# Optimization experiments

Hardware: AMD Instinct MI355X
Metric: run time of the kernel (lower is better)

Reference implementation:

```python
import jax, jax.numpy as jnp
import numpy as np

B, P, E = 128, 196, 2048      # batch, num_pixels (14x14), encoder_dim
A = D = EMB = 512             # attention_dim, decoder_dim, embed_dim
V = 18022                     # vocab_size
MAXLEN = 52                   # max caption length; decode steps T = MAXLEN-1


def _lin(key, fan_in, fan_out):
    k1, k2 = jax.random.split(key)
    s = 1.0 / np.sqrt(fan_in)
    W = jax.random.uniform(k1, (fan_in, fan_out), minval=-s, maxval=s, dtype=jnp.float32)
    b = jax.random.uniform(k2, (fan_out,), minval=-s, maxval=s, dtype=jnp.float32)
    return W, b


def setup_inputs() -> dict:
    key = jax.random.key(0)
    ks = jax.random.split(key, 14)
    W_enc_att, b_enc_att = _lin(ks[0], E, A)
    W_dec_att, b_dec_att = _lin(ks[1], D, A)
    w_full, b_full = _lin(ks[2], A, 1)
    W_init_h, b_init_h = _lin(ks[3], E, D)
    W_init_c, b_init_c = _lin(ks[4], E, D)
    W_fbeta, b_fbeta = _lin(ks[5], D, E)
    # LSTMCell params (torch layout: [4D, in] / [4D, D], gate order i,f,g,o)
    s = 1.0 / np.sqrt(D)
    W_ih = jax.random.uniform(ks[6], (4 * D, EMB + E), minval=-s, maxval=s, dtype=jnp.float32)
    W_hh = jax.random.uniform(ks[7], (4 * D, D), minval=-s, maxval=s, dtype=jnp.float32)
    b_ih = jax.random.uniform(ks[8], (4 * D,), minval=-s, maxval=s, dtype=jnp.float32)
    b_hh = jax.random.uniform(ks[9], (4 * D,), minval=-s, maxval=s, dtype=jnp.float32)
    # embedding and fc initialized uniform(-0.1, 0.1) per init_weights
    emb_table = jax.random.uniform(ks[10], (V, EMB), minval=-0.1, maxval=0.1, dtype=jnp.float32)
    W_fc = jax.random.uniform(ks[11], (D, V), minval=-0.1, maxval=0.1, dtype=jnp.float32)
    b_fc = jnp.zeros((V,), dtype=jnp.float32)

    encoder_out = jax.random.normal(ks[12], (B, P, E), dtype=jnp.float32)
    kc, kl = jax.random.split(ks[13])
    encoded_captions = jax.random.randint(kc, (B, MAXLEN), 0, V, dtype=jnp.int32)
    lengths = jax.random.randint(kl, (B,), 5, MAXLEN + 1, dtype=jnp.int32)
    caption_lengths = jnp.sort(lengths)[::-1].at[0].set(MAXLEN)  # descending, max = MAXLEN
    return {
        'encoder_out': encoder_out, 'encoded_captions': encoded_captions,
        'caption_lengths': caption_lengths, 'emb_table': emb_table,
        'W_enc_att': W_enc_att, 'b_enc_att': b_enc_att,
        'W_dec_att': W_dec_att, 'b_dec_att': b_dec_att,
        'w_full': w_full, 'b_full': b_full,
        'W_init_h': W_init_h, 'b_init_h': b_init_h,
        'W_init_c': W_init_c, 'b_init_c': b_init_c,
        'W_fbeta': W_fbeta, 'b_fbeta': b_fbeta,
        'W_ih': W_ih, 'b_ih': b_ih, 'W_hh': W_hh, 'b_hh': b_hh,
        'W_fc': W_fc, 'b_fc': b_fc,
    }


def reference(encoder_out, encoded_captions, caption_lengths, emb_table,
              W_enc_att, b_enc_att, W_dec_att, b_dec_att, w_full, b_full,
              W_init_h, b_init_h, W_init_c, b_init_c, W_fbeta, b_fbeta,
              W_ih, b_ih, W_hh, b_hh, W_fc, b_fc):
    T = encoded_captions.shape[1] - 1  # max decode length (lengths sorted desc, max=MAXLEN)
    emb = emb_table[encoded_captions]                 # [B, L, EMB]
    mean_enc = encoder_out.mean(axis=1)               # [B, E]
    h0 = mean_enc @ W_init_h + b_init_h               # [B, D]
    c0 = mean_enc @ W_init_c + b_init_c
    att1 = encoder_out @ W_enc_att + b_enc_att        # [B, P, A] (invariant over t)
    dec_len = caption_lengths - 1                     # [B]

    def step(carry, xs):
        h, c = carry
        emb_t, active = xs                            # [B, EMB], [B] bool
        att2 = h @ W_dec_att + b_dec_att              # [B, A]
        e = (jax.nn.relu(att1 + att2[:, None, :]) @ w_full)[..., 0] + b_full[0]  # [B, P]
        alpha = jax.nn.softmax(e, axis=1)
        awe = jnp.einsum('bpe,bp->be', encoder_out, alpha)   # [B, E]
        gate = jax.nn.sigmoid(h @ W_fbeta + b_fbeta)
        x = jnp.concatenate([emb_t, gate * awe], axis=1)     # [B, EMB+E]
        gates = x @ W_ih.T + b_ih + h @ W_hh.T + b_hh        # [B, 4D]
        i, f, g, o = jnp.split(gates, 4, axis=1)
        c_new = jax.nn.sigmoid(f) * c + jax.nn.sigmoid(i) * jnp.tanh(g)
        h_new = jax.nn.sigmoid(o) * jnp.tanh(c_new)
        preds = h_new @ W_fc + b_fc                          # [B, V] (dropout = identity in eval)
        m = active[:, None]
        h2 = jnp.where(m, h_new, h)                          # inactive rows keep old state
        c2 = jnp.where(m, c_new, c)
        return (h2, c2), (jnp.where(m, preds, 0.0), jnp.where(m, alpha, 0.0))

    active = jnp.arange(T)[:, None] < dec_len[None, :]       # [T, B]
    emb_in = jnp.swapaxes(emb[:, :T], 0, 1)                  # [T, B, EMB]
    _, (preds, alphas) = jax.lax.scan(step, (h0, c0), (emb_in, active))
    predictions = jnp.swapaxes(preds, 0, 1)                  # [B, T, V]
    alphas_out = jnp.swapaxes(alphas, 0, 1)                  # [B, T, P]
    return predictions, alphas_out
```

## Files before the change

kernel.cpp:

```cpp
#include <hip/hip_runtime.h>

typedef unsigned short u16;
typedef unsigned int u32;
typedef unsigned long long u64;
typedef __attribute__((ext_vector_type(8))) short short8;
typedef __attribute__((ext_vector_type(4))) float f32x4;
typedef __attribute__((ext_vector_type(4))) u32 u32x4;

#define DEV __device__ __forceinline__

DEV u16 f2b(float f) {
  u32 u = __builtin_bit_cast(u32, f);
  return (u16)((u + 0x7fffu + ((u >> 16) & 1u)) >> 16);
}
DEV float b2f(u16 h) { u32 u = (u32)h << 16; return __builtin_bit_cast(float, u); }
DEV float sigm(float x) { return 1.0f / (1.0f + __expf(-x)); }

template<int BM, int BN>
DEV void gemm_phase(const u16* __restrict__ A, const u16* __restrict__ Bt, int K,
                    u16* lA, u16* lB, int tid, int lane, int wm, int wn,
                    f32x4 (&acc)[BM/32][BN/32]) {
  constexpr int FM = BM / 32, FN = BN / 32;
  constexpr int CA = BM / 64, CB = BN / 64;
  for (int k0 = 0; k0 < K; k0 += 32) {
    u32x4 ra[CA], rb[CB];
#pragma unroll
    for (int c2 = 0; c2 < CA; ++c2) {
      int i = c2 * 256 + tid; int row = i >> 2; int col = (i & 3) * 8;
      ra[c2] = *(const u32x4*)(A + (u64)row * K + k0 + col);
    }
#pragma unroll
    for (int c2 = 0; c2 < CB; ++c2) {
      int i = c2 * 256 + tid; int row = i >> 2; int col = (i & 3) * 8;
      rb[c2] = *(const u32x4*)(Bt + (u64)row * K + k0 + col);
    }
    __syncthreads();
#pragma unroll
    for (int c2 = 0; c2 < CA; ++c2) { int i = c2 * 256 + tid; *(u32x4*)(lA + i * 8) = ra[c2]; }
#pragma unroll
    for (int c2 = 0; c2 < CB; ++c2) { int i = c2 * 256 + tid; *(u32x4*)(lB + i * 8) = rb[c2]; }
    __syncthreads();
    short8 af[FM], bfr[FN];
#pragma unroll
    for (int fm = 0; fm < FM; ++fm)
      af[fm] = *(const short8*)(lA + (wm * (BM / 2) + fm * 16 + (lane & 15)) * 32 + (lane >> 4) * 8);
#pragma unroll
    for (int fn = 0; fn < FN; ++fn)
      bfr[fn] = *(const short8*)(lB + (wn * (BN / 2) + fn * 16 + (lane & 15)) * 32 + (lane >> 4) * 8);
#pragma unroll
    for (int fm = 0; fm < FM; ++fm)
#pragma unroll
      for (int fn = 0; fn < FN; ++fn)
        acc[fm][fn] = __builtin_amdgcn_mfma_f32_16x16x32_bf16(af[fm], bfr[fn], acc[fm][fn], 0, 0, 0);
  }
}

template<int BM, int BN, int VAR>
__launch_bounds__(256)
__global__ void gemm_k(const u16* __restrict__ A, const u16* __restrict__ Bt, int K,
                       const u16* __restrict__ A2, const u16* __restrict__ Bt2, int K2,
                       int N,
                       const float* __restrict__ bias1, const float* __restrict__ bias2,
                       float* __restrict__ o1, float* __restrict__ o2,
                       u16* __restrict__ ob, const float* __restrict__ pre,
                       const int* __restrict__ caplen, int t) {
  constexpr int FM = BM / 32, FN = BN / 32;
  __shared__ __align__(16) u16 lA[BM * 32];
  __shared__ __align__(16) u16 lB[BN * 32];
  const int tid = threadIdx.x, lane = tid & 63;
  const int wm = (tid >> 6) >> 1, wn = (tid >> 6) & 1;
  const int m0 = blockIdx.x * BM, n0 = blockIdx.y * BN;
  f32x4 acc[FM][FN] = {};
  gemm_phase<BM, BN>(A + (u64)m0 * K, Bt + (u64)n0 * K, K, lA, lB, tid, lane, wm, wn, acc);
  if constexpr (VAR == 4) {
    gemm_phase<BM, BN>(A2 + (u64)m0 * K2, Bt2 + (u64)n0 * K2, K2, lA, lB, tid, lane, wm, wn, acc);
  }
#pragma unroll
  for (int fm = 0; fm < FM; ++fm) {
#pragma unroll
    for (int fn = 0; fn < FN; ++fn) {
#pragma unroll
      for (int r = 0; r < 4; ++r) {
        int m = m0 + wm * (BM / 2) + fm * 16 + ((lane >> 4) << 2) + r;
        int n = n0 + wn * (BN / 2) + fn * 16 + (lane & 15);
        float v = acc[fm][fn][r];
        if constexpr (VAR == 0) {
          ob[(u64)m * 512 + n] = f2b(v + bias1[n]);
        } else if constexpr (VAR == 1) {
          if (n < N) {
            int tt = m >> 7, b = m & 127;
            float val = (tt < caplen[b] - 1) ? (v + bias1[n]) : 0.0f;
            o1[((u64)b * 51 + tt) * 18022 + n] = val;
          }
        } else if constexpr (VAR == 2) {
          if (n < 512) o1[m * 512 + n] = v + bias1[n];
          else o2[m * 2048 + (n - 512)] = sigm(v + bias2[n - 512]);
        } else if constexpr (VAR == 3) {
          if (n < 512) ob[m * 512 + n] = f2b(v + bias1[n]);
          else o2[m * 512 + (n - 512)] = v + bias2[n - 512];
        } else if constexpr (VAR == 4) {
          o1[m * 2048 + n] = v + pre[(u64)m * 2048 + n];
        } else if constexpr (VAR == 5) {
          o1[(u64)m * 2048 + n] = v + bias1[n] + bias2[n];
        }
      }
    }
  }
}

__launch_bounds__(256)
__global__ void conv_cvt_k(u16* __restrict__ dst, const float* __restrict__ src,
                           int cols, int src_ld, int src_off) {
  int r = blockIdx.x;
  int c = blockIdx.y * 256 + threadIdx.x;
  if (c < cols) dst[(u64)r * cols + c] = f2b(src[(u64)r * src_ld + src_off + c]);
}

__launch_bounds__(256)
__global__ void transpose_cvt_k(u16* __restrict__ dst, const float* __restrict__ src, int R, int C) {
  __shared__ u16 tile[32][33];
  int c0 = blockIdx.x * 32, r0 = blockIdx.y * 32;
  int tx = threadIdx.x & 31, ty = threadIdx.x >> 5;
#pragma unroll
  for (int i = 0; i < 4; ++i) {
    int r = r0 + ty + i * 8, c = c0 + tx;
    u16 v = 0;
    if (r < R && c < C) v = f2b(src[(u64)r * C + c]);
    tile[ty + i * 8][tx] = v;
  }
  __syncthreads();
#pragma unroll
  for (int i = 0; i < 4; ++i) {
    int c = c0 + ty + i * 8, r = r0 + tx;
    if (c < C && r < R) dst[(u64)c * R + r] = tile[tx][ty + i * 8];
  }
}

__launch_bounds__(256)
__global__ void emb_gather_k(u16* __restrict__ dst, const float* __restrict__ table,
                             const int* __restrict__ caps) {
  int r = blockIdx.x;
  int c = blockIdx.y * 256 + threadIdx.x;
  int tt = r >> 7, b = r & 127;
  int tok = caps[b * 52 + tt];
  dst[(u64)r * 512 + c] = f2b(table[(u64)tok * 512 + c]);
}

__launch_bounds__(256)
__global__ void mean_k(u16* __restrict__ meanb, const u16* __restrict__ enc16) {
  int b = blockIdx.x;
  int e0 = (blockIdx.y * 256 + threadIdx.x) * 2;
  float s0 = 0.f, s1 = 0.f;
  const u16* p = enc16 + (u64)b * 196 * 2048 + e0;
  for (int pp = 0; pp < 196; ++pp) {
    u32 v = *(const u32*)(p + (u64)pp * 2048);
    s0 += b2f((u16)v); s1 += b2f((u16)(v >> 16));
  }
  const float inv = 1.0f / 196.0f;
  u32 o = (u32)f2b(s0 * inv) | ((u32)f2b(s1 * inv) << 16);
  *(u32*)(meanb + (u64)b * 2048 + e0) = o;
}

__launch_bounds__(256)
__global__ void alpha_k(const u16* __restrict__ att1, const float* __restrict__ att2,
                        const float* __restrict__ wfull,
                        float* __restrict__ alpha_ws, float* __restrict__ out_alpha,
                        const int* __restrict__ caplen, int t) {
  int b = blockIdx.x;
  __shared__ float s_e[196];
  __shared__ float s_red[8];
  int tid = threadIdx.x, lane = tid & 63, wave = tid >> 6;
  float a2r[8], wr[8];
  {
    const float* pa = att2 + b * 512 + lane * 8;
    const float* pw = wfull + lane * 8;
#pragma unroll
    for (int j = 0; j < 8; ++j) { a2r[j] = pa[j]; wr[j] = pw[j]; }
  }
  for (int p = wave; p < 196; p += 4) {
    const u16* row = att1 + ((u64)b * 196 + p) * 512 + lane * 8;
    u32x4 q = *(const u32x4*)row;
    float acc = 0.f;
#pragma unroll
    for (int j = 0; j < 4; ++j) {
      u32 w2 = q[j];
      float v0 = b2f((u16)w2) + a2r[2 * j];
      float v1 = b2f((u16)(w2 >> 16)) + a2r[2 * j + 1];
      acc += fmaxf(v0, 0.f) * wr[2 * j] + fmaxf(v1, 0.f) * wr[2 * j + 1];
    }
#pragma unroll
    for (int off = 32; off; off >>= 1) acc += __shfl_xor(acc, off);
    if (lane == 0) s_e[p] = acc;
  }
  __syncthreads();
  float v = (tid < 196) ? s_e[tid] : -1e30f;
  float mx = v;
#pragma unroll
  for (int off = 32; off; off >>= 1) mx = fmaxf(mx, __shfl_xor(mx, off));
  if (lane == 0) s_red[wave] = mx;
  __syncthreads();
  mx = fmaxf(fmaxf(s_red[0], s_red[1]), fmaxf(s_red[2], s_red[3]));
  float ex = (tid < 196) ? __expf(v - mx) : 0.f;
  float sm = ex;
#pragma unroll
  for (int off = 32; off; off >>= 1) sm += __shfl_xor(sm, off);
  if (lane == 0) s_red[4 + wave] = sm;
  __syncthreads();
  sm = s_red[4] + s_red[5] + s_red[6] + s_red[7];
  if (tid < 196) {
    float a = ex / sm;
    alpha_ws[b * 196 + tid] = a;
    bool act = t < caplen[b] - 1;
    out_alpha[((u64)b * 51 + t) * 196 + tid] = act ? a : 0.f;
  }
}

__launch_bounds__(256)
__global__ void awe_y_k(const u16* __restrict__ enc16, const float* __restrict__ alpha_ws,
                        const float* __restrict__ gate, u16* __restrict__ y) {
  int b = blockIdx.x;
  int e0 = blockIdx.y * 1024 + threadIdx.x * 4;
  __shared__ float s_a[196];
  for (int i = threadIdx.x; i < 196; i += 256) s_a[i] = alpha_ws[b * 196 + i];
  __syncthreads();
  float acc0 = 0, acc1 = 0, acc2 = 0, acc3 = 0;
  const u16* base = enc16 + (u64)b * 196 * 2048 + e0;
#pragma unroll 4
  for (int p = 0; p < 196; ++p) {
    const u16* q = base + (u64)p * 2048;
    u32 v0 = *(const u32*)q, v1 = *(const u32*)(q + 2);
    float ap = s_a[p];
    acc0 += ap * b2f((u16)v0); acc1 += ap * b2f((u16)(v0 >> 16));
    acc2 += ap * b2f((u16)v1); acc3 += ap * b2f((u16)(v1 >> 16));
  }
  const float* g = gate + b * 2048 + e0;
  u32 w0 = (u32)f2b(acc0 * g[0]) | ((u32)f2b(acc1 * g[1]) << 16);
  u32 w1 = (u32)f2b(acc2 * g[2]) | ((u32)f2b(acc3 * g[3]) << 16);
  *(u32*)(y + (u64)b * 2048 + e0) = w0;
  *(u32*)(y + (u64)b * 2048 + e0 + 2) = w1;
}

__launch_bounds__(256)
__global__ void lstm_k(const float* __restrict__ gates, float* __restrict__ c,
                       u16* __restrict__ hbf, u16* __restrict__ hall, int t) {
  int idx = blockIdx.x * 256 + threadIdx.x;
  int b = idx >> 9, d = idx & 511;
  const float* g = gates + b * 2048;
  float ig = g[d], fg = g[512 + d], gg = g[1024 + d], og = g[1536 + d];
  float cp = c[idx];
  float cn = sigm(fg) * cp + sigm(ig) * tanhf(gg);
  float hn = sigm(og) * tanhf(cn);
  c[idx] = cn;
  u16 hb = f2b(hn);
  hbf[idx] = hb;
  hall[((u64)t * 128 + b) * 512 + d] = hb;
}

extern "C" void kernel_launch(void* const* d_in, const int* in_sizes, int n_in,
                              void* d_out, int out_size, void* d_ws, size_t ws_size,
                              hipStream_t stream) {
  const float* enc    = (const float*)d_in[0];
  const int*   caps   = (const int*)d_in[1];
  const int*   caplen = (const int*)d_in[2];
  const float* embt   = (const float*)d_in[3];
  const float* Wenc   = (const float*)d_in[4];
  const float* benc   = (const float*)d_in[5];
  const float* Wdec   = (const float*)d_in[6];
  const float* bdec   = (const float*)d_in[7];
  const float* wfull  = (const float*)d_in[8];
  const float* Winh   = (const float*)d_in[10];
  const float* binh   = (const float*)d_in[11];
  const float* Winc   = (const float*)d_in[12];
  const float* binc   = (const float*)d_in[13];
  const float* Wfb    = (const float*)d_in[14];
  const float* bfb    = (const float*)d_in[15];
  const float* Wih    = (const float*)d_in[16];
  const float* bih    = (const float*)d_in[17];
  const float* Whh    = (const float*)d_in[18];
  const float* bhh    = (const float*)d_in[19];
  const float* Wfc    = (const float*)d_in[20];
  const float* bfc    = (const float*)d_in[21];
  float* out = (float*)d_out;
  float* out_alpha = out + 117647616ull;

  char* ws = (char*)d_ws;
  u16*   att1   = (u16*)(ws + 0);
  u16*   wenc_t = (u16*)(ws + 25690112);
  u16*   cat    = (u16*)(ws + 27787264);
  u16*   wihenc = (u16*)(ws + 32505856);
  u16*   wihemb = (u16*)(ws + 40894464);
  u16*   wfct   = (u16*)(ws + 42991616);
  u16*   winit  = (u16*)(ws + 61446144);
  u16*   embq   = (u16*)(ws + 65640448);
  float* pre    = (float*)(ws + 72325120);
  u16*   hall   = (u16*)(ws + 125802496);
  u16*   meanb  = (u16*)(ws + 132487168);
  float* cst    = (float*)(ws + 133011456);
  u16*   hbf    = (u16*)(ws + 133273600);
  float* att2   = (float*)(ws + 133404672);
  float* gateb  = (float*)(ws + 133666816);
  float* alphaw = (float*)(ws + 134715392);
  u16*   ybuf   = (u16*)(ws + 134815744);
  float* gates  = (float*)(ws + 135340032);
  u16*   enc16  = (u16*)(ws + 136388608);

  transpose_cvt_k<<<dim3(16, 64), 256, 0, stream>>>(wenc_t, Wenc, 2048, 512);
  transpose_cvt_k<<<dim3(16, 16), 256, 0, stream>>>(cat, Wdec, 512, 512);
  transpose_cvt_k<<<dim3(64, 16), 256, 0, stream>>>(cat + 512 * 512, Wfb, 512, 2048);
  conv_cvt_k<<<dim3(2048, 2), 256, 0, stream>>>(cat + 2560 * 512, Whh, 512, 512, 0);
  conv_cvt_k<<<dim3(2048, 8), 256, 0, stream>>>(wihenc, Wih, 2048, 2560, 512);
  conv_cvt_k<<<dim3(2048, 2), 256, 0, stream>>>(wihemb, Wih, 512, 2560, 0);
  transpose_cvt_k<<<dim3(564, 16), 256, 0, stream>>>(wfct, Wfc, 512, 18022);
  transpose_cvt_k<<<dim3(16, 64), 256, 0, stream>>>(winit, Winh, 2048, 512);
  transpose_cvt_k<<<dim3(16, 64), 256, 0, stream>>>(winit + 512 * 2048, Winc, 2048, 512);
  conv_cvt_k<<<dim3(25088, 8), 256, 0, stream>>>(enc16, enc, 2048, 2048, 0);
  emb_gather_k<<<dim3(6528, 2), 256, 0, stream>>>(embq, embt, caps);
  mean_k<<<dim3(128, 4), 256, 0, stream>>>(meanb, enc16);
  gemm_k<64, 64, 3><<<dim3(2, 16), 256, 0, stream>>>(
      meanb, winit, 2048, nullptr, nullptr, 0, 0, binh, binc,
      nullptr, cst, hbf, nullptr, nullptr, 0);
  gemm_k<128, 128, 0><<<dim3(196, 4), 256, 0, stream>>>(
      enc16, wenc_t, 2048, nullptr, nullptr, 0, 0, benc, nullptr,
      nullptr, nullptr, att1, nullptr, nullptr, 0);
  gemm_k<128, 128, 5><<<dim3(51, 16), 256, 0, stream>>>(
      embq, wihemb, 512, nullptr, nullptr, 0, 0, bih, bhh,
      pre, nullptr, nullptr, nullptr, nullptr, 0);

  for (int t = 0; t < 51; ++t) {
    gemm_k<64, 64, 2><<<dim3(2, 40), 256, 0, stream>>>(
        hbf, cat, 512, nullptr, nullptr, 0, 0, bdec, bfb,
        att2, gateb, nullptr, nullptr, nullptr, 0);
    alpha_k<<<128, 256, 0, stream>>>(att1, att2, wfull, alphaw, out_alpha, caplen, t);
    awe_y_k<<<dim3(128, 2), 256, 0, stream>>>(enc16, alphaw, gateb, ybuf);
    gemm_k<64, 64, 4><<<dim3(2, 32), 256, 0, stream>>>(
        ybuf, wihenc, 2048, hbf, cat + 2560 * 512, 512, 0, nullptr, nullptr,
        gates, nullptr, nullptr, pre + (u64)t * 128 * 2048, nullptr, 0);
    lstm_k<<<256, 256, 0, stream>>>(gates, cst, hbf, hall, t);
  }

  gemm_k<128, 128, 1><<<dim3(51, 141), 256, 0, stream>>>(
      hall, wfct, 512, nullptr, nullptr, 0, 18022, bfc, nullptr,
      out, nullptr, nullptr, nullptr, caplen, 0);
}
```

Before: 6.351 ms.

## Fuse per-step decode kernels into one persistent kernel with grid barriers

```diff
diff --git a/kernel.cpp b/kernel.cpp
--- a/kernel.cpp
+++ b/kernel.cpp
@@ -6,6 +6,7 @@
 typedef __attribute__((ext_vector_type(8))) short short8;
 typedef __attribute__((ext_vector_type(4))) float f32x4;
 typedef __attribute__((ext_vector_type(4))) u32 u32x4;
+typedef __attribute__((ext_vector_type(2))) u32 u32x2;
 
 #define DEV __device__ __forceinline__
 
@@ -22,24 +23,24 @@
                     f32x4 (&acc)[BM/32][BN/32]) {
   constexpr int FM = BM / 32, FN = BN / 32;
   constexpr int CA = BM / 64, CB = BN / 64;
+  u32x4 ra[CA], rb[CB];
+#pragma unroll
+  for (int c = 0; c < CA; ++c) { int i = c * 256 + tid; ra[c] = *(const u32x4*)(A + (u64)(i >> 2) * K + (i & 3) * 8); }
+#pragma unroll
+  for (int c = 0; c < CB; ++c) { int i = c * 256 + tid; rb[c] = *(const u32x4*)(Bt + (u64)(i >> 2) * K + (i & 3) * 8); }
   for (int k0 = 0; k0 < K; k0 += 32) {
-    u32x4 ra[CA], rb[CB];
-#pragma unroll
-    for (int c2 = 0; c2 < CA; ++c2) {
-      int i = c2 * 256 + tid; int row = i >> 2; int col = (i & 3) * 8;
-      ra[c2] = *(const u32x4*)(A + (u64)row * K + k0 + col);
-    }
-#pragma unroll
-    for (int c2 = 0; c2 < CB; ++c2) {
-      int i = c2 * 256 + tid; int row = i >> 2; int col = (i & 3) * 8;
-      rb[c2] = *(const u32x4*)(Bt + (u64)row * K + k0 + col);
-    }
     __syncthreads();
 #pragma unroll
-    for (int c2 = 0; c2 < CA; ++c2) { int i = c2 * 256 + tid; *(u32x4*)(lA + i * 8) = ra[c2]; }
-#pragma unroll
-    for (int c2 = 0; c2 < CB; ++c2) { int i = c2 * 256 + tid; *(u32x4*)(lB + i * 8) = rb[c2]; }
+    for (int c = 0; c < CA; ++c) { int i = c * 256 + tid; *(u32x4*)(lA + i * 8) = ra[c]; }
+#pragma unroll
+    for (int c = 0; c < CB; ++c) { int i = c * 256 + tid; *(u32x4*)(lB + i * 8) = rb[c]; }
     __syncthreads();
+    if (k0 + 32 < K) {
+#pragma unroll
+      for (int c = 0; c < CA; ++c) { int i = c * 256 + tid; ra[c] = *(const u32x4*)(A + (u64)(i >> 2) * K + k0 + 32 + (i & 3) * 8); }
+#pragma unroll
+      for (int c = 0; c < CB; ++c) { int i = c * 256 + tid; rb[c] = *(const u32x4*)(Bt + (u64)(i >> 2) * K + k0 + 32 + (i & 3) * 8); }
+    }
     short8 af[FM], bfr[FN];
 #pragma unroll
     for (int fm = 0; fm < FM; ++fm)
@@ -58,12 +59,11 @@
 template<int BM, int BN, int VAR>
 __launch_bounds__(256)
 __global__ void gemm_k(const u16* __restrict__ A, const u16* __restrict__ Bt, int K,
-                       const u16* __restrict__ A2, const u16* __restrict__ Bt2, int K2,
                        int N,
                        const float* __restrict__ bias1, const float* __restrict__ bias2,
                        float* __restrict__ o1, float* __restrict__ o2,
-                       u16* __restrict__ ob, const float* __restrict__ pre,
-                       const int* __restrict__ caplen, int t) {
+                       u16* __restrict__ ob,
+                       const int* __restrict__ caplen) {
   constexpr int FM = BM / 32, FN = BN / 32;
   __shared__ __align__(16) u16 lA[BM * 32];
   __shared__ __align__(16) u16 lB[BN * 32];
@@ -72,9 +72,6 @@
   const int m0 = blockIdx.x * BM, n0 = blockIdx.y * BN;
   f32x4 acc[FM][FN] = {};
   gemm_phase<BM, BN>(A + (u64)m0 * K, Bt + (u64)n0 * K, K, lA, lB, tid, lane, wm, wn, acc);
-  if constexpr (VAR == 4) {
-    gemm_phase<BM, BN>(A2 + (u64)m0 * K2, Bt2 + (u64)n0 * K2, K2, lA, lB, tid, lane, wm, wn, acc);
-  }
 #pragma unroll
   for (int fm = 0; fm < FM; ++fm) {
 #pragma unroll
@@ -92,28 +89,191 @@
             float val = (tt < caplen[b] - 1) ? (v + bias1[n]) : 0.0f;
             o1[((u64)b * 51 + tt) * 18022 + n] = val;
           }
-        } else if constexpr (VAR == 2) {
-          if (n < 512) o1[m * 512 + n] = v + bias1[n];
-          else o2[m * 2048 + (n - 512)] = sigm(v + bias2[n - 512]);
         } else if constexpr (VAR == 3) {
           if (n < 512) ob[m * 512 + n] = f2b(v + bias1[n]);
           else o2[m * 512 + (n - 512)] = v + bias2[n - 512];
-        } else if constexpr (VAR == 4) {
-          o1[m * 2048 + n] = v + pre[(u64)m * 2048 + n];
         } else if constexpr (VAR == 5) {
-          o1[(u64)m * 2048 + n] = v + bias1[n] + bias2[n];
+          int og = ((n & 3) << 9) | (n >> 2);
+          o1[(u64)m * 2048 + n] = v + bias1[og] + bias2[og];
         }
       }
     }
   }
 }
 
+DEV void gbar(u32* cnt, u32* gen, u32 target) {
+  __syncthreads();
+  if (threadIdx.x == 0) {
+    __threadfence();
+    u32 t = __hip_atomic_fetch_add(cnt, 1u, __ATOMIC_ACQ_REL, __HIP_MEMORY_SCOPE_AGENT);
+    if (t == gridDim.x - 1) {
+      __hip_atomic_store(cnt, 0u, __ATOMIC_RELAXED, __HIP_MEMORY_SCOPE_AGENT);
+      __hip_atomic_fetch_add(gen, 1u, __ATOMIC_RELEASE, __HIP_MEMORY_SCOPE_AGENT);
+    } else {
+      while (__hip_atomic_load(gen, __ATOMIC_ACQUIRE, __HIP_MEMORY_SCOPE_AGENT) < target)
+        __builtin_amdgcn_s_sleep(2);
+    }
+    __threadfence();
+  }
+  __syncthreads();
+}
+
+__launch_bounds__(256)
+__global__ void loop_k(const u16* __restrict__ att1, const u16* __restrict__ cat,
+                       const u16* __restrict__ wihenc, const float* __restrict__ pre,
+                       const u16* __restrict__ enc16,
+                       const float* __restrict__ bdec, const float* __restrict__ bfb,
+                       const float* __restrict__ wfull,
+                       float* __restrict__ att2g, float* __restrict__ gateg,
+                       u16* __restrict__ ybuf,
+                       float* __restrict__ cst, u16* __restrict__ hbf0, u16* __restrict__ hbf1,
+                       u16* __restrict__ hall, float* __restrict__ out_alpha,
+                       const int* __restrict__ caplen, u32* __restrict__ bar) {
+  __shared__ __align__(16) char smem[16384];
+  const int bid = blockIdx.x, tid = threadIdx.x, lane = tid & 63;
+  const int wm = (tid >> 6) >> 1, wn = (tid >> 6) & 1;
+  u32* cnt = bar; u32* gen = bar + 32;
+  u32 bgen = 0;
+  u16* hc = hbf0; u16* hnx = hbf1;
+
+  for (int t = 0; t < 51; ++t) {
+    if (bid < 80) {
+      u16* lA = (u16*)smem; u16* lB = lA + 64 * 32;
+      int m0 = (bid & 1) * 64, n0 = (bid >> 1) * 64;
+      f32x4 acc[2][2] = {};
+      gemm_phase<64, 64>(hc + (u64)m0 * 512, cat + (u64)n0 * 512, 512, lA, lB, tid, lane, wm, wn, acc);
+#pragma unroll
+      for (int fm = 0; fm < 2; ++fm)
+#pragma unroll
+        for (int fn = 0; fn < 2; ++fn)
+#pragma unroll
+          for (int r = 0; r < 4; ++r) {
+            int m = m0 + wm * 32 + fm * 16 + ((lane >> 4) << 2) + r;
+            int n = n0 + wn * 32 + fn * 16 + (lane & 15);
+            float v = acc[fm][fn][r];
+            if (n < 512) att2g[m * 512 + n] = v + bdec[n];
+            else gateg[m * 2048 + (n - 512)] = sigm(v + bfb[n - 512]);
+          }
+    }
+    gbar(cnt, gen, ++bgen);
+
+    {
+      int b = bid >> 1, half = bid & 1;
+      float* s_e = (float*)smem;
+      float* s_red = s_e + 196;
+      float* s_al = s_red + 8;
+      float a2r[8], wr[8];
+      {
+        const float* pa = att2g + b * 512 + lane * 8;
+        const float* pw = wfull + lane * 8;
+#pragma unroll
+        for (int j = 0; j < 8; ++j) { a2r[j] = pa[j]; wr[j] = pw[j]; }
+      }
+      int wave = tid >> 6;
+      for (int p = wave; p < 196; p += 4) {
+        const u16* row = att1 + ((u64)b * 196 + p) * 512 + lane * 8;
+        u32x4 q = *(const u32x4*)row;
+        float acc = 0.f;
+#pragma unroll
+        for (int j = 0; j < 4; ++j) {
+          u32 w2 = q[j];
+          float v0 = b2f((u16)w2) + a2r[2 * j];
+          float v1 = b2f((u16)(w2 >> 16)) + a2r[2 * j + 1];
+          acc += fmaxf(v0, 0.f) * wr[2 * j] + fmaxf(v1, 0.f) * wr[2 * j + 1];
+        }
+#pragma unroll
+        for (int off = 32; off; off >>= 1) acc += __shfl_xor(acc, off);
+        if (lane == 0) s_e[p] = acc;
+      }
+      __syncthreads();
+      float v = (tid < 196) ? s_e[tid] : -1e30f;
+      float mx = v;
+#pragma unroll
+      for (int off = 32; off; off >>= 1) mx = fmaxf(mx, __shfl_xor(mx, off));
+      if (lane == 0) s_red[wave] = mx;
+      __syncthreads();
+      mx = fmaxf(fmaxf(s_red[0], s_red[1]), fmaxf(s_red[2], s_red[3]));
+      float ex = (tid < 196) ? __expf(v - mx) : 0.f;
+      float sm = ex;
+#pragma unroll
+      for (int off = 32; off; off >>= 1) sm += __shfl_xor(sm, off);
+      if (lane == 0) s_red[4 + wave] = sm;
+      __syncthreads();
+      sm = s_red[4] + s_red[5] + s_red[6] + s_red[7];
+      if (tid < 196) s_al[tid] = ex / sm;
+      __syncthreads();
+      if (half == 0 && tid < 196) {
+        bool act = t < caplen[b] - 1;
+        out_alpha[((u64)b * 51 + t) * 196 + tid] = act ? s_al[tid] : 0.f;
+      }
+      float aw0 = 0, aw1 = 0, aw2 = 0, aw3 = 0;
+      const u16* base = enc16 + (u64)b * 196 * 2048 + half * 1024 + tid * 4;
+#pragma unroll 4
+      for (int p = 0; p < 196; ++p) {
+        u32x2 q = *(const u32x2*)(base + (u64)p * 2048);
+        float ap = s_al[p];
+        aw0 += ap * b2f((u16)q[0]); aw1 += ap * b2f((u16)(q[0] >> 16));
+        aw2 += ap * b2f((u16)q[1]); aw3 += ap * b2f((u16)(q[1] >> 16));
+      }
+      const float* gr = gateg + b * 2048 + half * 1024 + tid * 4;
+      u32 w0 = (u32)f2b(aw0 * gr[0]) | ((u32)f2b(aw1 * gr[1]) << 16);
+      u32 w1 = (u32)f2b(aw2 * gr[2]) | ((u32)f2b(aw3 * gr[3]) << 16);
+      u16* yp = ybuf + b * 2048 + half * 1024 + tid * 4;
+      *(u32*)yp = w0; *(u32*)(yp + 2) = w1;
+    }
+    gbar(cnt, gen, ++bgen);
+
+    if (bid < 64) {
+      u16* lA = (u16*)smem; u16* lB = lA + 64 * 32;
+      int m0 = (bid & 1) * 64, n0 = (bid >> 1) * 64;
+      f32x4 acc[2][2] = {};
+      gemm_phase<64, 64>(ybuf + (u64)m0 * 2048, wihenc + (u64)n0 * 2048, 2048, lA, lB, tid, lane, wm, wn, acc);
+      gemm_phase<64, 64>(hc + (u64)m0 * 512, cat + (u64)2560 * 512 + (u64)n0 * 512, 512, lA, lB, tid, lane, wm, wn, acc);
+      __syncthreads();
+      float* gbuf = (float*)smem;
+      const float* prow = pre + ((u64)t * 128 + m0) * 2048 + n0;
+#pragma unroll
+      for (int fm = 0; fm < 2; ++fm)
+#pragma unroll
+        for (int fn = 0; fn < 2; ++fn)
+#pragma unroll
+          for (int r = 0; r < 4; ++r) {
+            int ml = wm * 32 + fm * 16 + ((lane >> 4) << 2) + r;
+            int nl = wn * 32 + fn * 16 + (lane & 15);
+            gbuf[ml * 64 + nl] = acc[fm][fn][r] + prow[(u64)ml * 2048 + nl];
+          }
+      __syncthreads();
+#pragma unroll
+      for (int j = 0; j < 4; ++j) {
+        int l = tid + 256 * j;
+        int lm = l >> 4, ld = l & 15;
+        int b = m0 + lm, d = (n0 >> 2) + ld;
+        const float* gq = gbuf + lm * 64 + ld * 4;
+        float ig = gq[0], fg = gq[1], gg = gq[2], og = gq[3];
+        float cp = cst[b * 512 + d];
+        float cn = sigm(fg) * cp + sigm(ig) * tanhf(gg);
+        float hv = sigm(og) * tanhf(cn);
+        cst[b * 512 + d] = cn;
+        u16 hb = f2b(hv);
+        hnx[b * 512 + d] = hb;
+        hall[((u64)t * 128 + b) * 512 + d] = hb;
+      }
+    }
+    gbar(cnt, gen, ++bgen);
+    u16* tmp = hc; hc = hnx; hnx = tmp;
+  }
+}
+
+__launch_bounds__(64)
+__global__ void init_bar_k(u32* bar) { bar[threadIdx.x] = 0; }
+
 __launch_bounds__(256)
 __global__ void conv_cvt_k(u16* __restrict__ dst, const float* __restrict__ src,
-                           int cols, int src_ld, int src_off) {
+                           int cols, int src_ld, int src_off, int ileave) {
   int r = blockIdx.x;
   int c = blockIdx.y * 256 + threadIdx.x;
-  if (c < cols) dst[(u64)r * cols + c] = f2b(src[(u64)r * src_ld + src_off + c]);
+  int rd = ileave ? ((r & 511) * 4 + (r >> 9)) : r;
+  if (c < cols) dst[(u64)rd * cols + c] = f2b(src[(u64)r * src_ld + src_off + c]);
 }
 
 __launch_bounds__(256)
@@ -159,101 +319,6 @@
   const float inv = 1.0f / 196.0f;
   u32 o = (u32)f2b(s0 * inv) | ((u32)f2b(s1 * inv) << 16);
   *(u32*)(meanb + (u64)b * 2048 + e0) = o;
-}
-
-__launch_bounds__(256)
-__global__ void alpha_k(const u16* __restrict__ att1, const float* __restrict__ att2,
-                        const float* __restrict__ wfull,
-                        float* __restrict__ alpha_ws, float* __restrict__ out_alpha,
-                        const int* __restrict__ caplen, int t) {
-  int b = blockIdx.x;
-  __shared__ float s_e[196];
-  __shared__ float s_red[8];
-  int tid = threadIdx.x, lane = tid & 63, wave = tid >> 6;
-  float a2r[8], wr[8];
-  {
-    const float* pa = att2 + b * 512 + lane * 8;
-    const float* pw = wfull + lane * 8;
-#pragma unroll
-    for (int j = 0; j < 8; ++j) { a2r[j] = pa[j]; wr[j] = pw[j]; }
-  }
-  for (int p = wave; p < 196; p += 4) {
-    const u16* row = att1 + ((u64)b * 196 + p) * 512 + lane * 8;
-    u32x4 q = *(const u32x4*)row;
-    float acc = 0.f;
-#pragma unroll
-    for (int j = 0; j < 4; ++j) {
-      u32 w2 = q[j];
-      float v0 = b2f((u16)w2) + a2r[2 * j];
-      float v1 = b2f((u16)(w2 >> 16)) + a2r[2 * j + 1];
-      acc += fmaxf(v0, 0.f) * wr[2 * j] + fmaxf(v1, 0.f) * wr[2 * j + 1];
-    }
-#pragma unroll
-    for (int off = 32; off; off >>= 1) acc += __shfl_xor(acc, off);
-    if (lane == 0) s_e[p] = acc;
-  }
-  __syncthreads();
-  float v = (tid < 196) ? s_e[tid] : -1e30f;
-  float mx = v;
-#pragma unroll
-  for (int off = 32; off; off >>= 1) mx = fmaxf(mx, __shfl_xor(mx, off));
-  if (lane == 0) s_red[wave] = mx;
-  __syncthreads();
-  mx = fmaxf(fmaxf(s_red[0], s_red[1]), fmaxf(s_red[2], s_red[3]));
-  float ex = (tid < 196) ? __expf(v - mx) : 0.f;
-  float sm = ex;
-#pragma unroll
-  for (int off = 32; off; off >>= 1) sm += __shfl_xor(sm, off);
-  if (lane == 0) s_red[4 + wave] = sm;
-  __syncthreads();
-  sm = s_red[4] + s_red[5] + s_red[6] + s_red[7];
-  if (tid < 196) {
-    float a = ex / sm;
-    alpha_ws[b * 196 + tid] = a;
-    bool act = t < caplen[b] - 1;
-    out_alpha[((u64)b * 51 + t) * 196 + tid] = act ? a : 0.f;
-  }
-}
-
-__launch_bounds__(256)
-__global__ void awe_y_k(const u16* __restrict__ enc16, const float* __restrict__ alpha_ws,
-                        const float* __restrict__ gate, u16* __restrict__ y) {
-  int b = blockIdx.x;
-  int e0 = blockIdx.y * 1024 + threadIdx.x * 4;
-  __shared__ float s_a[196];
-  for (int i = threadIdx.x; i < 196; i += 256) s_a[i] = alpha_ws[b * 196 + i];
-  __syncthreads();
-  float acc0 = 0, acc1 = 0, acc2 = 0, acc3 = 0;
-  const u16* base = enc16 + (u64)b * 196 * 2048 + e0;
-#pragma unroll 4
-  for (int p = 0; p < 196; ++p) {
-    const u16* q = base + (u64)p * 2048;
-    u32 v0 = *(const u32*)q, v1 = *(const u32*)(q + 2);
-    float ap = s_a[p];
-    acc0 += ap * b2f((u16)v0); acc1 += ap * b2f((u16)(v0 >> 16));
-    acc2 += ap * b2f((u16)v1); acc3 += ap * b2f((u16)(v1 >> 16));
-  }
-  const float* g = gate + b * 2048 + e0;
-  u32 w0 = (u32)f2b(acc0 * g[0]) | ((u32)f2b(acc1 * g[1]) << 16);
-  u32 w1 = (u32)f2b(acc2 * g[2]) | ((u32)f2b(acc3 * g[3]) << 16);
-  *(u32*)(y + (u64)b * 2048 + e0) = w0;
-  *(u32*)(y + (u64)b * 2048 + e0 + 2) = w1;
-}
-
-__launch_bounds__(256)
-__global__ void lstm_k(const float* __restrict__ gates, float* __restrict__ c,
-                       u16* __restrict__ hbf, u16* __restrict__ hall, int t) {
-  int idx = blockIdx.x * 256 + threadIdx.x;
-  int b = idx >> 9, d = idx & 511;
-  const float* g = gates + b * 2048;
-  float ig = g[d], fg = g[512 + d], gg = g[1024 + d], og = g[1536 + d];
-  float cp = c[idx];
-  float cn = sigm(fg) * cp + sigm(ig) * tanhf(gg);
-  float hn = sigm(og) * tanhf(cn);
-  c[idx] = cn;
-  u16 hb = f2b(hn);
-  hbf[idx] = hb;
-  hall[((u64)t * 128 + b) * 512 + d] = hb;
 }
 
 extern "C" void kernel_launch(void* const* d_in, const int* in_sizes, int n_in,
@@ -296,49 +361,38 @@
   u16*   hall   = (u16*)(ws + 125802496);
   u16*   meanb  = (u16*)(ws + 132487168);
   float* cst    = (float*)(ws + 133011456);
-  u16*   hbf    = (u16*)(ws + 133273600);
-  float* att2   = (float*)(ws + 133404672);
-  float* gateb  = (float*)(ws + 133666816);
-  float* alphaw = (float*)(ws + 134715392);
-  u16*   ybuf   = (u16*)(ws + 134815744);
-  float* gates  = (float*)(ws + 135340032);
-  u16*   enc16  = (u16*)(ws + 136388608);
-
+  u16*   hbf0   = (u16*)(ws + 133273600);
+  u16*   hbf1   = (u16*)(ws + 133404672);
+  float* att2g  = (float*)(ws + 133535744);
+  float* gateg  = (float*)(ws + 133797888);
+  u16*   ybuf   = (u16*)(ws + 134846464);
+  u32*   bar    = (u32*)(ws + 135370752);
+  u16*   enc16  = (u16*)(ws + 135371264);
+
+  init_bar_k<<<1, 64, 0, stream>>>(bar);
   transpose_cvt_k<<<dim3(16, 64), 256, 0, stream>>>(wenc_t, Wenc, 2048, 512);
   transpose_cvt_k<<<dim3(16, 16), 256, 0, stream>>>(cat, Wdec, 512, 512);
   transpose_cvt_k<<<dim3(64, 16), 256, 0, stream>>>(cat + 512 * 512, Wfb, 512, 2048);
-  conv_cvt_k<<<dim3(2048, 2), 256, 0, stream>>>(cat + 2560 * 512, Whh, 512, 512, 0);
-  conv_cvt_k<<<dim3(2048, 8), 256, 0, stream>>>(wihenc, Wih, 2048, 2560, 512);
-  conv_cvt_k<<<dim3(2048, 2), 256, 0, stream>>>(wihemb, Wih, 512, 2560, 0);
+  conv_cvt_k<<<dim3(2048, 2), 256, 0, stream>>>(cat + 2560 * 512, Whh, 512, 512, 0, 1);
+  conv_cvt_k<<<dim3(2048, 8), 256, 0, stream>>>(wihenc, Wih, 2048, 2560, 512, 1);
+  conv_cvt_k<<<dim3(2048, 2), 256, 0, stream>>>(wihemb, Wih, 512, 2560, 0, 1);
   transpose_cvt_k<<<dim3(564, 16), 256, 0, stream>>>(wfct, Wfc, 512, 18022);
   transpose_cvt_k<<<dim3(16, 64), 256, 0, stream>>>(winit, Winh, 2048, 512);
   transpose_cvt_k<<<dim3(16, 64), 256, 0, stream>>>(winit + 512 * 2048, Winc, 2048, 512);
-  conv_cvt_k<<<dim3(25088, 8), 256, 0, stream>>>(enc16, enc, 2048, 2048, 0);
+  conv_cvt_k<<<dim3(25088, 8), 256, 0, stream>>>(enc16, enc, 2048, 2048, 0, 0);
   emb_gather_k<<<dim3(6528, 2), 256, 0, stream>>>(embq, embt, caps);
   mean_k<<<dim3(128, 4), 256, 0, stream>>>(meanb, enc16);
   gemm_k<64, 64, 3><<<dim3(2, 16), 256, 0, stream>>>(
-      meanb, winit, 2048, nullptr, nullptr, 0, 0, binh, binc,
-      nullptr, cst, hbf, nullptr, nullptr, 0);
+      meanb, winit, 2048, 0, binh, binc, nullptr, cst, hbf0, nullptr);
   gemm_k<128, 128, 0><<<dim3(196, 4), 256, 0, stream>>>(
-      enc16, wenc_t, 2048, nullptr, nullptr, 0, 0, benc, nullptr,
-      nullptr, nullptr, att1, nullptr, nullptr, 0);
+      enc16, wenc_t, 2048, 0, benc, nullptr, nullptr, nullptr, att1, nullptr);
   gemm_k<128, 128, 5><<<dim3(51, 16), 256, 0, stream>>>(
-      embq, wihemb, 512, nullptr, nullptr, 0, 0, bih, bhh,
-      pre, nullptr, nullptr, nullptr, nullptr, 0);
-
-  for (int t = 0; t < 51; ++t) {
-    gemm_k<64, 64, 2><<<dim3(2, 40), 256, 0, stream>>>(
-        hbf, cat, 512, nullptr, nullptr, 0, 0, bdec, bfb,
-        att2, gateb, nullptr, nullptr, nullptr, 0);
-    alpha_k<<<128, 256, 0, stream>>>(att1, att2, wfull, alphaw, out_alpha, caplen, t);
-    awe_y_k<<<dim3(128, 2), 256, 0, stream>>>(enc16, alphaw, gateb, ybuf);
-    gemm_k<64, 64, 4><<<dim3(2, 32), 256, 0, stream>>>(
-        ybuf, wihenc, 2048, hbf, cat + 2560 * 512, 512, 0, nullptr, nullptr,
-        gates, nullptr, nullptr, pre + (u64)t * 128 * 2048, nullptr, 0);
-    lstm_k<<<256, 256, 0, stream>>>(gates, cst, hbf, hall, t);
-  }
+      embq, wihemb, 512, 0, bih, bhh, pre, nullptr, nullptr, nullptr);
+
+  loop_k<<<256, 256, 0, stream>>>(att1, cat, wihenc, pre, enc16, bdec, bfb, wfull,
+                                  att2g, gateg, ybuf, cst, hbf0, hbf1, hall,
+                                  out_alpha, caplen, bar);
 
   gemm_k<128, 128, 1><<<dim3(51, 141), 256, 0, stream>>>(
-      hall, wfct, 512, nullptr, nullptr, 0, 18022, bfc, nullptr,
-      out, nullptr, nullptr, nullptr, caplen, 0);
-}
+      hall, wfct, 512, 18022, bfc, nullptr, out, nullptr, nullptr, caplen);
+}
```

New measurement: 14.58 ms. +129.6%, slower.
